# Kernel optimization log

Hardware: AMD Instinct MI355X
Metric: run time of the kernel (lower is better)

Reference implementation:

```python
import jax, jax.numpy as jnp
import numpy as np

VOCAB, EMB, HID, SEQ = 8000, 512, 1024, 1024


def _gru_step(h, x, wih, whh, bih, bhh):
    # h: (1,H), x: (1,E). PyTorch GRUCell math.
    gi = x @ wih.T + bih          # (1,3H)
    gh = h @ whh.T + bhh          # (1,3H)
    ir, iz, inn = jnp.split(gi, 3, axis=-1)
    hr, hz, hn = jnp.split(gh, 3, axis=-1)
    r = jax.nn.sigmoid(ir + hr)
    z = jax.nn.sigmoid(iz + hz)
    n = jnp.tanh(inn + r * hn)
    return (1.0 - z) * n + z * h


def setup_inputs() -> dict:
    key = jax.random.key(0)
    ks = jax.random.split(key, 16)
    s = 0.05
    return {
        "char_seq": jax.random.randint(ks[0], (SEQ,), 0, VOCAB),
        "target_char_seq": jax.random.randint(ks[1], (SEQ,), 0, VOCAB),
        "enc_state": jax.random.normal(ks[2], (1, 1, HID), jnp.float32) * s,
        "emb_table": jax.random.normal(ks[3], (VOCAB, EMB), jnp.float32) * s,
        "enc_wih": jax.random.normal(ks[4], (3 * HID, EMB), jnp.float32) * s,
        "enc_whh": jax.random.normal(ks[5], (3 * HID, HID), jnp.float32) * s,
        "enc_bih": jax.random.normal(ks[6], (3 * HID,), jnp.float32) * s,
        "enc_bhh": jax.random.normal(ks[7], (3 * HID,), jnp.float32) * s,
        "dec_wih": jax.random.normal(ks[8], (3 * HID, EMB), jnp.float32) * s,
        "dec_whh": jax.random.normal(ks[9], (3 * HID, HID), jnp.float32) * s,
        "dec_bih": jax.random.normal(ks[10], (3 * HID,), jnp.float32) * s,
        "dec_bhh": jax.random.normal(ks[11], (3 * HID,), jnp.float32) * s,
        "out_w": jax.random.normal(ks[12], (VOCAB, HID), jnp.float32) * s,
        "out_b": jax.random.normal(ks[13], (VOCAB,), jnp.float32) * s,
        "sos_id": 1,
        "eos_id": 2,
        "sep_id": 3,
        "max_out_char_seq_len": SEQ,
    }


def reference(char_seq, target_char_seq, enc_state, emb_table,
              enc_wih, enc_whh, enc_bih, enc_bhh,
              dec_wih, dec_whh, dec_bih, dec_bhh,
              out_w, out_b, sos_id, eos_id, sep_id, max_out_char_seq_len):
    # ---- encode: GRU over nonzero chars only (masked state update keeps shapes static) ----
    h = enc_state.reshape(1, -1)               # (1,H)
    x_enc = emb_table[char_seq]                # (L,E)
    mask = (char_seq != 0)

    def enc_body(h, xm):
        xe, m = xm
        hn = _gru_step(h, xe[None, :], enc_wih, enc_whh, enc_bih, enc_bhh)
        return jnp.where(m, hn, h), None

    h, _ = jax.lax.scan(enc_body, h, (x_enc, mask))

    # ---- decode: teacher forcing; input at step t is sos for t=0 else target[t-1] ----
    sos = jnp.full((1,), sos_id, dtype=target_char_seq.dtype)
    dec_in = jnp.concatenate([sos, target_char_seq[:-1]])
    x_dec = emb_table[dec_in]                  # (T,E)

    def dec_body(h, xe):
        hn = _gru_step(h, xe[None, :], dec_wih, dec_whh, dec_bih, dec_bhh)
        score = hn @ out_w.T + out_b           # (1,V)
        return hn, (score[0], hn[0])

    _, (scores, states) = jax.lax.scan(dec_body, h, x_dec)  # (T,V), (T,H)

    # early-stop on eos: step t is emitted iff no target[j]==eos for j<t (step where
    # target[t]==eos is still emitted, then loop breaks); remaining steps are zero-padded.
    ne = (target_char_seq != eos_id).astype(scores.dtype)
    valid = jnp.concatenate([jnp.ones((1,), scores.dtype), jnp.cumprod(ne)[:-1]])
    char_scores_out = (scores * valid[:, None])[None]   # (1,T,V)
    char_states_out = (states * valid[:, None])[None]   # (1,T,H)
    return char_scores_out, char_states_out
```

## Files before the change

### kernel.cpp

```cpp
#include <hip/hip_runtime.h>
#include <math.h>

#define VOCAB 8000
#define EMB   512
#define HID   1024
#define SEQ_L 1024
#define G3    (3*HID)
#define NWG   64
#define POISON 0xAAAAAAAAu
#define RLX __ATOMIC_RELAXED
#define AGT __HIP_MEMORY_SCOPE_AGENT

typedef float v2f __attribute__((ext_vector_type(2)));
typedef float v4f __attribute__((ext_vector_type(4)));

__device__ __forceinline__ v4f ic_load4(const float* p) {
  v4f r;
  asm volatile("global_load_dwordx4 %0, %1, off sc0 sc1\n\ts_waitcnt vmcnt(0)"
               : "=v"(r) : "v"(p) : "memory");
  return r;
}
__device__ __forceinline__ bool any_poison4(v4f v) {
  return __float_as_uint(v.x) == POISON || __float_as_uint(v.y) == POISON ||
         __float_as_uint(v.z) == POISON || __float_as_uint(v.w) == POISON;
}
__device__ __forceinline__ void publishf(float* p, float v) {
  if (__float_as_uint(v) == POISON) v = __uint_as_float(POISON ^ 1u);
  atomicExch(p, v);
}
__device__ __forceinline__ float row16_sum(float x) {
  int v = __float_as_int(x);
  x += __int_as_float(__builtin_amdgcn_update_dpp(0, v, 0xB1,  0xF, 0xF, false)); v = __float_as_int(x);
  x += __int_as_float(__builtin_amdgcn_update_dpp(0, v, 0x4E,  0xF, 0xF, false)); v = __float_as_int(x);
  x += __int_as_float(__builtin_amdgcn_update_dpp(0, v, 0x141, 0xF, 0xF, false)); v = __float_as_int(x);
  x += __int_as_float(__builtin_amdgcn_update_dpp(0, v, 0x140, 0xF, 0xF, false));
  return x;
}

__global__ __launch_bounds__(1024) void prep_kernel(
    const int* __restrict__ target, const int* __restrict__ sos_p,
    const int* __restrict__ eos_p, int* __restrict__ dec_in,
    float* __restrict__ valid)
{
  int t = threadIdx.x;
  int eos = eos_p[0];
  dec_in[t] = (t == 0) ? sos_p[0] : target[t - 1];
  bool ne = (target[t] != eos);
  unsigned long long b = __ballot(ne);
  int lane = t & 63, w = t >> 6;
  __shared__ unsigned long long wb[16];
  if (lane == 0) wb[w] = b;
  __syncthreads();
  bool ok = (((~b) & ((1ull << lane) - 1ull)) == 0ull);
  for (int i = 0; i < 16; i++)
    if (i < w) ok = ok && (wb[i] == ~0ull);
  valid[t] = ok ? 1.0f : 0.0f;
}

__global__ __launch_bounds__(256) void gemm_nt(
    const float* __restrict__ A, const int* __restrict__ idx,
    const float* __restrict__ B, const float* __restrict__ bias,
    const float* __restrict__ rowscale, float* __restrict__ C,
    int M, int N, int K)
{
  __shared__ __align__(16) float As[16][132];
  __shared__ __align__(16) float Bs[16][132];
  const int tid = threadIdx.x;
  const int bm = blockIdx.y * 128;
  const int bn = blockIdx.x * 128;
  const int tx = tid & 15, ty = tid >> 4;
  float acc[8][8];
#pragma unroll
  for (int i = 0; i < 8; i++)
#pragma unroll
    for (int jj = 0; jj < 8; jj++) acc[i][jj] = 0.f;

  for (int k0 = 0; k0 < K; k0 += 16) {
    __syncthreads();
#pragma unroll
    for (int r = 0; r < 2; r++) {
      int v = tid + 256 * r;
      int row = v >> 2;
      int kq = (v & 3) << 2;
      int m = bm + row;
      const float* abase = idx ? (A + (size_t)idx[m] * K) : (A + (size_t)m * K);
      float4 av = *(const float4*)(abase + k0 + kq);
      As[kq + 0][row] = av.x; As[kq + 1][row] = av.y;
      As[kq + 2][row] = av.z; As[kq + 3][row] = av.w;
      int n = bn + row;
      float4 bv = make_float4(0.f, 0.f, 0.f, 0.f);
      if (n < N) bv = *(const float4*)(B + (size_t)n * K + k0 + kq);
      Bs[kq + 0][row] = bv.x; Bs[kq + 1][row] = bv.y;
      Bs[kq + 2][row] = bv.z; Bs[kq + 3][row] = bv.w;
    }
    __syncthreads();
#pragma unroll
    for (int k = 0; k < 16; k++) {
      float am[8], bb[8];
      *(float4*)&am[0] = *(const float4*)&As[k][ty * 8];
      *(float4*)&am[4] = *(const float4*)&As[k][ty * 8 + 4];
      *(float4*)&bb[0] = *(const float4*)&Bs[k][tx * 8];
      *(float4*)&bb[4] = *(const float4*)&Bs[k][tx * 8 + 4];
#pragma unroll
      for (int i = 0; i < 8; i++)
#pragma unroll
        for (int jj = 0; jj < 8; jj++)
          acc[i][jj] += am[i] * bb[jj];
    }
  }
#pragma unroll
  for (int i = 0; i < 8; i++) {
    int m = bm + ty * 8 + i;
    float rs = rowscale ? rowscale[m] : 1.0f;
#pragma unroll
    for (int jj = 0; jj < 8; jj++) {
      int n = bn + tx * 8 + jj;
      if (n < N) C[(size_t)m * N + n] = (acc[i][jj] + bias[n]) * rs;
    }
  }
}

__global__ __launch_bounds__(1024, 1) void recur_kernel(
    const float* __restrict__ enc_whh, const float* __restrict__ enc_bhh,
    const float* __restrict__ dec_whh, const float* __restrict__ dec_bhh,
    const float* __restrict__ enc_state, const int* __restrict__ char_seq,
    const float* __restrict__ gi_enc, const float* __restrict__ gi_dec,
    float* hbuf)
{
  const int wg   = blockIdx.x;
  const int tid  = threadIdx.x;
  const int lane = tid & 63;
  const int w    = tid >> 6;
  const int j    = wg * 16 + w;

  __shared__ __align__(16) float hLDS[HID];

  if (lane == 0) publishf(&hbuf[j], enc_state[j]);
  if (tid >= 960 && tid < 976)
    atomicOr((unsigned int*)&hbuf[(size_t)(tid - 959) * HID + wg * 16], 0u);

  v2f wv[3][8];
#pragma unroll
  for (int g = 0; g < 3; g++) {
    const float* wrow = enc_whh + (size_t)(g * HID + j) * HID + lane * 16;
#pragma unroll
    for (int u = 0; u < 4; u++) {
      v4f t4 = *(const v4f*)(wrow + u * 4);
      wv[g][2 * u]     = (v2f){t4.x, t4.y};
      wv[g][2 * u + 1] = (v2f){t4.z, t4.w};
    }
  }
  float bhr = enc_bhh[j], bhz = enc_bhh[HID + j], bhn = enc_bhh[2 * HID + j];

  for (int s = 1; s <= 2 * SEQ_L; s++) {
    if (s == SEQ_L + 1) {
#pragma unroll
      for (int g = 0; g < 3; g++) {
        const float* wrow = dec_whh + (size_t)(g * HID + j) * HID + lane * 16;
#pragma unroll
        for (int u = 0; u < 4; u++) {
          v4f t4 = *(const v4f*)(wrow + u * 4);
          wv[g][2 * u]     = (v2f){t4.x, t4.y};
          wv[g][2 * u + 1] = (v2f){t4.z, t4.w};
        }
      }
      bhr = dec_bhh[j]; bhz = dec_bhh[HID + j]; bhn = dec_bhh[2 * HID + j];
    }
    if (tid == 976 && s + 16 <= 2 * SEQ_L)
      atomicOr((unsigned int*)&hbuf[(size_t)(s + 16) * HID + wg * 16], 0u);

    float gir = 0.f, giz = 0.f, gin = 0.f;
    int cs = 1;
    if (lane == 0) {
      const float* gi = (s <= SEQ_L) ? (gi_enc + (size_t)(s - 1) * G3)
                                     : (gi_dec + (size_t)(s - SEQ_L - 1) * G3);
      gir = gi[j]; giz = gi[HID + j]; gin = gi[2 * HID + j];
      if (s <= SEQ_L) cs = char_seq[s - 1];
    }
    if (tid < 256) {
      const float* hp = hbuf + (size_t)(s - 1) * HID + 4 * tid;
      v4f hv = ic_load4(hp);
      while (any_poison4(hv)) hv = ic_load4(hp);
      int us = tid ^ ((tid >> 3) & 7);
      *(v4f*)&hLDS[us * 4] = hv;
    }
    __syncthreads();
    int uj = j >> 2, usj = uj ^ ((uj >> 3) & 7);
    float hold = hLDS[usj * 4 + (j & 3)];
    v2f acc2[3] = {(v2f){0.f, 0.f}, (v2f){0.f, 0.f}, (v2f){0.f, 0.f}};
#pragma unroll
    for (int u = 0; u < 4; u++) {
      int uu = lane * 4 + u, s2 = uu ^ ((uu >> 3) & 7);
      v4f hv = *(const v4f*)&hLDS[s2 * 4];
      v2f h0 = (v2f){hv.x, hv.y}, h1 = (v2f){hv.z, hv.w};
#pragma unroll
      for (int g = 0; g < 3; g++) {
        acc2[g] = __builtin_elementwise_fma(wv[g][2 * u], h0, acc2[g]);
        acc2[g] = __builtin_elementwise_fma(wv[g][2 * u + 1], h1, acc2[g]);
      }
    }
    float gh[3];
#pragma unroll
    for (int g = 0; g < 3; g++) {
      float t = row16_sum(acc2[g].x + acc2[g].y);
      t += __shfl_xor(t, 16, 64);
      t += __shfl_xor(t, 32, 64);
      gh[g] = t;
    }
    if (lane == 0) {
      float ghr = gh[0] + bhr, ghz = gh[1] + bhz, ghn = gh[2] + bhn;
      float r = __builtin_amdgcn_rcpf(1.f + __expf(-(gir + ghr)));
      float z = __builtin_amdgcn_rcpf(1.f + __expf(-(giz + ghz)));
      float x = gin + r * ghn;
      float e = __expf(2.f * x);
      float n = 1.f - 2.f * __builtin_amdgcn_rcpf(e + 1.f);
      float hnew = (1.f - z) * n + z * hold;
      if (s <= SEQ_L && cs == 0) hnew = hold;
      publishf(&hbuf[(size_t)s * HID + j], hnew);
    }
  }
}

__global__ __launch_bounds__(256) void states_kernel(
    const float* __restrict__ hdec, const float* __restrict__ valid,
    float* __restrict__ out2)
{
  int i = blockIdx.x * 256 + threadIdx.x;
  out2[i] = hdec[i] * valid[i >> 10];
}

extern "C" void kernel_launch(void* const* d_in, const int* in_sizes, int n_in,
                              void* d_out, int out_size, void* d_ws, size_t ws_size,
                              hipStream_t stream)
{
  const int*   char_seq  = (const int*)  d_in[0];
  const int*   target    = (const int*)  d_in[1];
  const float* enc_state = (const float*)d_in[2];
  const float* emb       = (const float*)d_in[3];
  const float* enc_wih   = (const float*)d_in[4];
  const float* enc_whh   = (const float*)d_in[5];
  const float* enc_bih   = (const float*)d_in[6];
  const float* enc_bhh   = (const float*)d_in[7];
  const float* dec_wih   = (const float*)d_in[8];
  const float* dec_whh   = (const float*)d_in[9];
  const float* dec_bih   = (const float*)d_in[10];
  const float* dec_bhh   = (const float*)d_in[11];
  const float* out_w     = (const float*)d_in[12];
  const float* out_b     = (const float*)d_in[13];
  const int*   sos_p     = (const int*)  d_in[14];
  const int*   eos_p     = (const int*)  d_in[15];

  char* ws = (char*)d_ws;
  float* gi_enc = (float*)ws;  ws += (size_t)SEQ_L * G3 * sizeof(float);
  float* gi_dec = (float*)ws;  ws += (size_t)SEQ_L * G3 * sizeof(float);
  float* hbuf   = (float*)ws;  ws += (size_t)(2 * SEQ_L + 1) * HID * sizeof(float);
  float* valid  = (float*)ws;  ws += SEQ_L * sizeof(float);
  int*   dec_in = (int*)ws;    ws += SEQ_L * sizeof(int);

  float* hdec = hbuf + (size_t)(SEQ_L + 1) * HID;

  float* out_scores = (float*)d_out;
  float* out_states = out_scores + (size_t)SEQ_L * VOCAB;

  prep_kernel<<<1, 1024, 0, stream>>>(target, sos_p, eos_p, dec_in, valid);
  gemm_nt<<<dim3(G3 / 128, SEQ_L / 128), 256, 0, stream>>>(
      emb, char_seq, enc_wih, enc_bih, nullptr, gi_enc, SEQ_L, G3, EMB);
  gemm_nt<<<dim3(G3 / 128, SEQ_L / 128), 256, 0, stream>>>(
      emb, dec_in, dec_wih, dec_bih, nullptr, gi_dec, SEQ_L, G3, EMB);
  recur_kernel<<<NWG, 1024, 0, stream>>>(
      enc_whh, enc_bhh, dec_whh, dec_bhh, enc_state, char_seq,
      gi_enc, gi_dec, hbuf);
  gemm_nt<<<dim3((VOCAB + 127) / 128, SEQ_L / 128), 256, 0, stream>>>(
      hdec, nullptr, out_w, out_b, valid, out_scores, SEQ_L, VOCAB, HID);
  states_kernel<<<(SEQ_L * HID) / 256, 256, 0, stream>>>(hdec, valid, out_states);
}
```

Baseline: 4.225 ms.

## Poll hidden state via pipelined global_load_lds into LDS ring buffer

Replaces the blocking spin on coherent global loads of the previous hidden state with asynchronous global-to-LDS loads that keep several requests in flight. Each poll reads the LDS slot, which is pre-filled with poison, and exits once no lane sees poison. A triple-buffered LDS ring and a spin limit that falls back to the old ic_load4 path are added. The aim is to cut per-step inter-workgroup synchronization latency in the serial GRU recurrence. The cost is extra LDS, more complex memory ordering, and the risk of reading stale data if cache-policy bits or waitcnt handling are wrong.

```diff
diff --git a/kernel.cpp b/kernel.cpp
--- a/kernel.cpp
+++ b/kernel.cpp
@@ -8,8 +8,6 @@
 #define G3    (3*HID)
 #define NWG   64
 #define POISON 0xAAAAAAAAu
-#define RLX __ATOMIC_RELAXED
-#define AGT __HIP_MEMORY_SCOPE_AGENT
 
 typedef float v2f __attribute__((ext_vector_type(2)));
 typedef float v4f __attribute__((ext_vector_type(4)));
@@ -134,6 +132,7 @@
   const int j    = wg * 16 + w;
 
   __shared__ __align__(16) float hLDS[HID];
+  __shared__ __align__(16) float pollbuf[3][HID];
 
   if (lane == 0) publishf(&hbuf[j], enc_state[j]);
   if (tid >= 960 && tid < 976)
@@ -152,7 +151,11 @@
   }
   float bhr = enc_bhh[j], bhz = enc_bhh[HID + j], bhn = enc_bhh[2 * HID + j];
 
+  bool fb = false;
+  int  par = 0;
+
   for (int s = 1; s <= 2 * SEQ_L; s++) {
+    par = (par == 2) ? 0 : par + 1;
     if (s == SEQ_L + 1) {
 #pragma unroll
       for (int g = 0; g < 3; g++) {
@@ -177,10 +180,34 @@
       gir = gi[j]; giz = gi[HID + j]; gin = gi[2 * HID + j];
       if (s <= SEQ_L) cs = char_seq[s - 1];
     }
+
     if (tid < 256) {
+      float* slot = &pollbuf[par][4 * tid];
+      float* ldsbase = &pollbuf[par][(tid >> 6) * 256];
       const float* hp = hbuf + (size_t)(s - 1) * HID + 4 * tid;
-      v4f hv = ic_load4(hp);
-      while (any_poison4(hv)) hv = ic_load4(hp);
+      v4f hv;
+      bool got = false;
+      if (!fb) {
+        float pz = __uint_as_float(POISON);
+        *(volatile v4f*)slot = (v4f){pz, pz, pz, pz};
+        int spins = 0;
+        for (;;) {
+          asm volatile("s_waitcnt vmcnt(3)" ::: "memory");
+          v4f t = *(volatile const v4f*)slot;
+          if (!__any(any_poison4(t))) {
+            hv = t;
+            got = true;
+            break;
+          }
+          if (++spins == 4096) { fb = true; break; }
+          __builtin_amdgcn_global_load_lds(hp, ldsbase, 16, 0, 17 );
+        }
+      }
+      if (!got) {
+        v4f t = ic_load4(hp);
+        while (any_poison4(t)) t = ic_load4(hp);
+        hv = t;
+      }
       int us = tid ^ ((tid >> 3) & 7);
       *(v4f*)&hLDS[us * 4] = hv;
     }
```

New measurement: 4.295 ms. About the same (+1.6%).
